# Kernel optimization log

Measured on AMD Instinct MI355X. Metric: run time of the kernel, lower is better.

## Reference

```python
import jax, jax.numpy as jnp
import numpy as np

B, D, C = 16384, 512, 1000  # batch, feature dim, number of class prototypes


def setup_inputs() -> dict:
    key = jax.random.key(0)
    kx, kp = jax.random.split(key)
    x = jax.random.normal(kx, (B, D), dtype=jnp.float32)
    protomat = jax.random.normal(kp, (C, D), dtype=jnp.float32)
    return {"x": x, "protomat": protomat}


def reference(x, protomat):
    # Squared L2 distance from every sample to every prototype:
    # dist[b, c] = sum_d (x[b,d] - protomat[c,d])^2
    # materializing the [B, C, D] broadcast the original loop implies.
    x_sq = jnp.sum(x * x, axis=1, keepdims=True)            # [B, 1]
    p_sq = jnp.sum(protomat * protomat, axis=1)             # [C]
    cross = jnp.einsum('bd,cd->bc', x, protomat)            # [B, C]
    return x_sq + p_sq[None, :] - 2.0 * cross               # [B, C]
```

## Files before the change

kernel.cpp:

```cpp
#include <hip/hip_runtime.h>
#include <hip/hip_bf16.h>


#define B_ROWS 16384
#define D_K    512
#define C_COLS 1000
#define C_PAD  1024

#define BM 128
#define BN 128
#define BK 32

typedef __attribute__((ext_vector_type(8))) short short8;
typedef __attribute__((ext_vector_type(4))) float f32x4;

__device__ __forceinline__ unsigned short f2bf(float f) {
  unsigned u = __float_as_uint(f);
  u += 0x7fffu + ((u >> 16) & 1u);
  return (unsigned short)(u >> 16);
}

__device__ __forceinline__ void gload16(const void* g, void* l) {
  __builtin_amdgcn_global_load_lds(
      (const __attribute__((address_space(1))) unsigned int*)g,
      (__attribute__((address_space(3))) unsigned int*)l, 16, 0, 0);
}

__global__ __launch_bounds__(256) void prep_kernel(
    const float* __restrict__ x, const float* __restrict__ p,
    unsigned short* __restrict__ xb, unsigned short* __restrict__ pb,
    float* __restrict__ xsq, float* __restrict__ psq) {
  const int wave = threadIdx.x >> 6;
  const int lane = threadIdx.x & 63;
  const int row  = blockIdx.x * 4 + wave;
  const bool isx = row < B_ROWS;
  const int r2   = isx ? row : row - B_ROWS;

  float v[8];
  if (isx) {
    const float4* s = reinterpret_cast<const float4*>(x + (size_t)r2 * D_K + lane * 8);
    float4 a = s[0], b = s[1];
    v[0] = a.x; v[1] = a.y; v[2] = a.z; v[3] = a.w;
    v[4] = b.x; v[5] = b.y; v[6] = b.z; v[7] = b.w;
  } else if (r2 < C_COLS) {
    const float4* s = reinterpret_cast<const float4*>(p + (size_t)r2 * D_K + lane * 8);
    float4 a = s[0], b = s[1];
    v[0] = a.x; v[1] = a.y; v[2] = a.z; v[3] = a.w;
    v[4] = b.x; v[5] = b.y; v[6] = b.z; v[7] = b.w;
  } else {
#pragma unroll
    for (int j = 0; j < 8; ++j) v[j] = 0.0f;
  }

  float ss = 0.0f;
  unsigned short u[8];
#pragma unroll
  for (int j = 0; j < 8; ++j) { ss += v[j] * v[j]; u[j] = f2bf(v[j]); }

  uint4 pk;
  pk.x = (unsigned)u[0] | ((unsigned)u[1] << 16);
  pk.y = (unsigned)u[2] | ((unsigned)u[3] << 16);
  pk.z = (unsigned)u[4] | ((unsigned)u[5] << 16);
  pk.w = (unsigned)u[6] | ((unsigned)u[7] << 16);
  unsigned short* dst = (isx ? xb : pb) + (size_t)r2 * D_K + lane * 8;
  *reinterpret_cast<uint4*>(dst) = pk;

#pragma unroll
  for (int off = 32; off > 0; off >>= 1) ss += __shfl_down(ss, off);
  if (lane == 0) (isx ? xsq : psq)[r2] = ss;
}

__global__ __launch_bounds__(256, 2) void gemm_kernel(
    const unsigned short* __restrict__ xb, const unsigned short* __restrict__ pb,
    const float* __restrict__ xsq, const float* __restrict__ psq,
    float* __restrict__ out) {
  __shared__ __align__(16) unsigned short As[BM * BK];
  __shared__ __align__(16) unsigned short Bs[BN * BK];

  const int tid  = threadIdx.x;
  const int lane = tid & 63;
  const int wave = tid >> 6;
  const int wr   = wave >> 1;
  const int wc   = wave & 1;
  const int bm   = blockIdx.y;
  const int bn   = blockIdx.x;

  const int ch0 = tid;
  const int ch1 = tid + 256;
  const unsigned short* a0 = xb + ((size_t)bm * BM + (ch0 >> 2)) * D_K + (ch0 & 3) * 8;
  const unsigned short* a1 = xb + ((size_t)bm * BM + (ch1 >> 2)) * D_K + (ch1 & 3) * 8;
  const unsigned short* b0 = pb + ((size_t)bn * BN + (ch0 >> 2)) * D_K + (ch0 & 3) * 8;
  const unsigned short* b1 = pb + ((size_t)bn * BN + (ch1 >> 2)) * D_K + (ch1 & 3) * 8;
  unsigned short* la0 = &As[ch0 * 8];
  unsigned short* la1 = &As[ch1 * 8];
  unsigned short* lb0 = &Bs[ch0 * 8];
  unsigned short* lb1 = &Bs[ch1 * 8];

  f32x4 acc[4][4];
#pragma unroll
  for (int i = 0; i < 4; ++i)
#pragma unroll
    for (int j = 0; j < 4; ++j) acc[i][j] = (f32x4){0.f, 0.f, 0.f, 0.f};

  const int mrow = wr * 64 + (lane & 15);
  const int ncol = wc * 64 + (lane & 15);
  const int koff = (lane >> 4) * 8;

#pragma unroll 1
  for (int ks = 0; ks < D_K / BK; ++ks) {
    const int ko = ks * BK;
    gload16(a0 + ko, la0);
    gload16(a1 + ko, la1);
    gload16(b0 + ko, lb0);
    gload16(b1 + ko, lb1);
    __syncthreads();

    short8 af[4], bf[4];
#pragma unroll
    for (int i = 0; i < 4; ++i)
      af[i] = *reinterpret_cast<const short8*>(&As[(mrow + i * 16) * BK + koff]);
#pragma unroll
    for (int j = 0; j < 4; ++j)
      bf[j] = *reinterpret_cast<const short8*>(&Bs[(ncol + j * 16) * BK + koff]);

#pragma unroll
    for (int i = 0; i < 4; ++i)
#pragma unroll
      for (int j = 0; j < 4; ++j)
        acc[i][j] = __builtin_amdgcn_mfma_f32_16x16x32_bf16(af[i], bf[j], acc[i][j], 0, 0, 0);

    __syncthreads();
  }

  const int colbase = bn * BN + wc * 64 + (lane & 15);
  float pc[4];
#pragma unroll
  for (int j = 0; j < 4; ++j) pc[j] = psq[colbase + j * 16];

  const int rowbase = bm * BM + wr * 64 + ((lane >> 4) << 2);
#pragma unroll
  for (int i = 0; i < 4; ++i) {
#pragma unroll
    for (int r = 0; r < 4; ++r) {
      const int row = rowbase + i * 16 + r;
      const float xs = xsq[row];
#pragma unroll
      for (int j = 0; j < 4; ++j) {
        const int c = colbase + j * 16;
        if (c < C_COLS)
          out[(size_t)row * C_COLS + c] = xs + pc[j] - 2.0f * acc[i][j][r];
      }
    }
  }
}

extern "C" void kernel_launch(void* const* d_in, const int* in_sizes, int n_in,
                              void* d_out, int out_size, void* d_ws, size_t ws_size,
                              hipStream_t stream) {
  const float* x = (const float*)d_in[0];
  const float* p = (const float*)d_in[1];
  float* out = (float*)d_out;

  char* ws = (char*)d_ws;
  unsigned short* xb  = (unsigned short*)ws;
  unsigned short* pb  = (unsigned short*)(ws + 16777216);
  float* xsq          = (float*)(ws + 16777216 + 1048576);
  float* psq          = (float*)(ws + 16777216 + 1048576 + 65536);

  prep_kernel<<<(B_ROWS + C_PAD) / 4, 256, 0, stream>>>(x, p, xb, pb, xsq, psq);

  dim3 grid(C_PAD / BN, B_ROWS / BM, 1);
  gemm_kernel<<<grid, 256, 0, stream>>>(xb, pb, xsq, psq, out);
}
```

Before: 123.4 us.

## Fuse bf16 conversion and norms into a single double-buffered 256x256 GEMM kernel

Drops the separate prep kernel and workspace round-trip. The GEMM now loads fp32 x and prototypes straight from global memory into registers, converts them to bf16, accumulates squared norms on the fly and writes swizzled LDS tiles through a register-prefetched double buffer. Tiles grow to 256x256 with 512 threads, and the grid is a remapped 1D grid of 256 blocks. In exchange, the prototype operand is converted redundantly in every block, occupancy drops to one large block per CU, and only 256 blocks are launched.

```diff
diff --git a/kernel.cpp b/kernel.cpp
--- a/kernel.cpp
+++ b/kernel.cpp
@@ -5,150 +5,141 @@
 #define B_ROWS 16384
 #define D_K    512
 #define C_COLS 1000
-#define C_PAD  1024
 
-#define BM 128
-#define BN 128
+#define BM 256
+#define BN 256
 #define BK 32
+#define NTL (D_K / BK)
 
 typedef __attribute__((ext_vector_type(8))) short short8;
 typedef __attribute__((ext_vector_type(4))) float f32x4;
 
-__device__ __forceinline__ unsigned short f2bf(float f) {
-  unsigned u = __float_as_uint(f);
-  u += 0x7fffu + ((u >> 16) & 1u);
-  return (unsigned short)(u >> 16);
+__device__ __forceinline__ f32x4 MFMA(short8 a, short8 b, f32x4 c) {
+  return __builtin_amdgcn_mfma_f32_16x16x32_bf16(a, b, c, 0, 0, 0);
 }
 
-__device__ __forceinline__ void gload16(const void* g, void* l) {
-  __builtin_amdgcn_global_load_lds(
-      (const __attribute__((address_space(1))) unsigned int*)g,
-      (__attribute__((address_space(3))) unsigned int*)l, 16, 0, 0);
-}
-
-__global__ __launch_bounds__(256) void prep_kernel(
+__global__ __launch_bounds__(512, 1) void fused_kernel(
     const float* __restrict__ x, const float* __restrict__ p,
-    unsigned short* __restrict__ xb, unsigned short* __restrict__ pb,
-    float* __restrict__ xsq, float* __restrict__ psq) {
-  const int wave = threadIdx.x >> 6;
-  const int lane = threadIdx.x & 63;
-  const int row  = blockIdx.x * 4 + wave;
-  const bool isx = row < B_ROWS;
-  const int r2   = isx ? row : row - B_ROWS;
-
-  float v[8];
-  if (isx) {
-    const float4* s = reinterpret_cast<const float4*>(x + (size_t)r2 * D_K + lane * 8);
-    float4 a = s[0], b = s[1];
-    v[0] = a.x; v[1] = a.y; v[2] = a.z; v[3] = a.w;
-    v[4] = b.x; v[5] = b.y; v[6] = b.z; v[7] = b.w;
-  } else if (r2 < C_COLS) {
-    const float4* s = reinterpret_cast<const float4*>(p + (size_t)r2 * D_K + lane * 8);
-    float4 a = s[0], b = s[1];
-    v[0] = a.x; v[1] = a.y; v[2] = a.z; v[3] = a.w;
-    v[4] = b.x; v[5] = b.y; v[6] = b.z; v[7] = b.w;
-  } else {
-#pragma unroll
-    for (int j = 0; j < 8; ++j) v[j] = 0.0f;
-  }
-
-  float ss = 0.0f;
-  unsigned short u[8];
-#pragma unroll
-  for (int j = 0; j < 8; ++j) { ss += v[j] * v[j]; u[j] = f2bf(v[j]); }
-
-  uint4 pk;
-  pk.x = (unsigned)u[0] | ((unsigned)u[1] << 16);
-  pk.y = (unsigned)u[2] | ((unsigned)u[3] << 16);
-  pk.z = (unsigned)u[4] | ((unsigned)u[5] << 16);
-  pk.w = (unsigned)u[6] | ((unsigned)u[7] << 16);
-  unsigned short* dst = (isx ? xb : pb) + (size_t)r2 * D_K + lane * 8;
-  *reinterpret_cast<uint4*>(dst) = pk;
-
-#pragma unroll
-  for (int off = 32; off > 0; off >>= 1) ss += __shfl_down(ss, off);
-  if (lane == 0) (isx ? xsq : psq)[r2] = ss;
-}
-
-__global__ __launch_bounds__(256, 2) void gemm_kernel(
-    const unsigned short* __restrict__ xb, const unsigned short* __restrict__ pb,
-    const float* __restrict__ xsq, const float* __restrict__ psq,
     float* __restrict__ out) {
-  __shared__ __align__(16) unsigned short As[BM * BK];
-  __shared__ __align__(16) unsigned short Bs[BN * BK];
+  __shared__ __align__(16) unsigned short L[2 * 16384];
+  __shared__ float SQ[512];
 
   const int tid  = threadIdx.x;
   const int lane = tid & 63;
   const int wave = tid >> 6;
-  const int wr   = wave >> 1;
-  const int wc   = wave & 1;
-  const int bm   = blockIdx.y;
-  const int bn   = blockIdx.x;
+  const int wm   = wave >> 2;
+  const int wn   = wave & 3;
 
-  const int ch0 = tid;
-  const int ch1 = tid + 256;
-  const unsigned short* a0 = xb + ((size_t)bm * BM + (ch0 >> 2)) * D_K + (ch0 & 3) * 8;
-  const unsigned short* a1 = xb + ((size_t)bm * BM + (ch1 >> 2)) * D_K + (ch1 & 3) * 8;
-  const unsigned short* b0 = pb + ((size_t)bn * BN + (ch0 >> 2)) * D_K + (ch0 & 3) * 8;
-  const unsigned short* b1 = pb + ((size_t)bn * BN + (ch1 >> 2)) * D_K + (ch1 & 3) * 8;
-  unsigned short* la0 = &As[ch0 * 8];
-  unsigned short* la1 = &As[ch1 * 8];
-  unsigned short* lb0 = &Bs[ch0 * 8];
-  unsigned short* lb1 = &Bs[ch1 * 8];
+  const int bid = blockIdx.x;
+  const int tt  = (bid & 7) * 32 + (bid >> 3);
+  const int bm  = tt >> 2;
+  const int bn  = tt & 3;
 
-  f32x4 acc[4][4];
+  const int rloc = tid & 255;
+  const float* gsrc;
+  if (tid < 256) {
+    gsrc = x + (size_t)(bm * BM + rloc) * D_K;
+  } else {
+    int prow = bn * BN + rloc;
+    if (prow > C_COLS - 1) prow = C_COLS - 1;
+    gsrc = p + (size_t)prow * D_K;
+  }
+  unsigned short* lreg = L + (tid < 256 ? 0 : 8192);
+  const int rsh = (rloc >> 1) & 3;
+
+  float ssq = 0.f;
+  float4 RA[8], RB[8];
+
+  auto GLOAD = [&](float4* R, int T) {
+    const float4* s = reinterpret_cast<const float4*>(gsrc + T * BK);
 #pragma unroll
-  for (int i = 0; i < 4; ++i)
+    for (int j = 0; j < 8; ++j) R[j] = s[j];
+  };
+
+  auto CVTW = [&](const float4* R, int BUF) {
+    __hip_bfloat162 h[16];
 #pragma unroll
-    for (int j = 0; j < 4; ++j) acc[i][j] = (f32x4){0.f, 0.f, 0.f, 0.f};
+    for (int j = 0; j < 8; ++j) {
+      ssq += R[j].x * R[j].x + R[j].y * R[j].y + R[j].z * R[j].z +
+             R[j].w * R[j].w;
+      h[2 * j]     = __float22bfloat162_rn(float2{R[j].x, R[j].y});
+      h[2 * j + 1] = __float22bfloat162_rn(float2{R[j].z, R[j].w});
+    }
+    const uint4* hu = reinterpret_cast<const uint4*>(h);
+    unsigned short* base = lreg + BUF * 16384;
+#pragma unroll
+    for (int ks = 0; ks < 4; ++ks) {
+      const int chunk = rloc * 4 + ((ks + rsh) & 3);
+      *reinterpret_cast<uint4*>(base + chunk * 8) = hu[ks];
+    }
+  };
 
-  const int mrow = wr * 64 + (lane & 15);
-  const int ncol = wc * 64 + (lane & 15);
-  const int koff = (lane >> 4) * 8;
+  f32x4 acc[8][4];
+#pragma unroll
+  for (int m = 0; m < 8; ++m)
+#pragma unroll
+    for (int n = 0; n < 4; ++n) acc[m][n] = (f32x4){0.f, 0.f, 0.f, 0.f};
+
+  const int l15  = lane & 15;
+  const int posL = (((lane >> 4) + (l15 >> 1)) & 3);
+  const int rdA  = (wm * 128 + l15) * 32 + posL * 8;
+  const int rdB  = 8192 + (wn * 64 + l15) * 32 + posL * 8;
+
+  auto COMPUTE = [&](int BUF) {
+    const unsigned short* Ab = &L[BUF * 16384] + rdA;
+    const unsigned short* Bb = &L[BUF * 16384] + rdB;
+    short8 bfr[4];
+#pragma unroll
+    for (int n = 0; n < 4; ++n)
+      bfr[n] = *reinterpret_cast<const short8*>(Bb + n * 512);
+    __builtin_amdgcn_s_setprio(1);
+#pragma unroll
+    for (int m = 0; m < 8; ++m) {
+      short8 af = *reinterpret_cast<const short8*>(Ab + m * 512);
+#pragma unroll
+      for (int n = 0; n < 4; ++n) acc[m][n] = MFMA(af, bfr[n], acc[m][n]);
+    }
+    __builtin_amdgcn_s_setprio(0);
+  };
+
+  GLOAD(RA, 0);
+  GLOAD(RB, 1);
+  CVTW(RA, 0);
+  __syncthreads();
 
 #pragma unroll 1
-  for (int ks = 0; ks < D_K / BK; ++ks) {
-    const int ko = ks * BK;
-    gload16(a0 + ko, la0);
-    gload16(a1 + ko, la1);
-    gload16(b0 + ko, lb0);
-    gload16(b1 + ko, lb1);
+  for (int t = 0; t < NTL; t += 2) {
+    if (t + 2 < NTL) GLOAD(RA, t + 2);
+    COMPUTE(0);
+    CVTW(RB, 1);
     __syncthreads();
-
-    short8 af[4], bf[4];
-#pragma unroll
-    for (int i = 0; i < 4; ++i)
-      af[i] = *reinterpret_cast<const short8*>(&As[(mrow + i * 16) * BK + koff]);
-#pragma unroll
-    for (int j = 0; j < 4; ++j)
-      bf[j] = *reinterpret_cast<const short8*>(&Bs[(ncol + j * 16) * BK + koff]);
-
-#pragma unroll
-    for (int i = 0; i < 4; ++i)
-#pragma unroll
-      for (int j = 0; j < 4; ++j)
-        acc[i][j] = __builtin_amdgcn_mfma_f32_16x16x32_bf16(af[i], bf[j], acc[i][j], 0, 0, 0);
-
+    if (t + 3 < NTL) GLOAD(RB, t + 3);
+    COMPUTE(1);
+    if (t + 2 < NTL) CVTW(RA, 0);
     __syncthreads();
   }
 
-  const int colbase = bn * BN + wc * 64 + (lane & 15);
+  SQ[tid] = ssq;
+  __syncthreads();
+
+  const int col_l = wn * 64 + l15;
   float pc[4];
 #pragma unroll
-  for (int j = 0; j < 4; ++j) pc[j] = psq[colbase + j * 16];
+  for (int n = 0; n < 4; ++n) pc[n] = SQ[256 + col_l + n * 16];
 
-  const int rowbase = bm * BM + wr * 64 + ((lane >> 4) << 2);
+  const int row_l0 = wm * 128 + ((lane >> 4) << 2);
+  const int gcol0  = bn * BN + col_l;
 #pragma unroll
-  for (int i = 0; i < 4; ++i) {
+  for (int m = 0; m < 8; ++m) {
 #pragma unroll
     for (int r = 0; r < 4; ++r) {
-      const int row = rowbase + i * 16 + r;
-      const float xs = xsq[row];
+      const int row_l = row_l0 + m * 16 + r;
+      const float xs  = SQ[row_l];
+      const size_t gr = (size_t)(bm * BM + row_l) * C_COLS;
 #pragma unroll
-      for (int j = 0; j < 4; ++j) {
-        const int c = colbase + j * 16;
-        if (c < C_COLS)
-          out[(size_t)row * C_COLS + c] = xs + pc[j] - 2.0f * acc[i][j][r];
+      for (int n = 0; n < 4; ++n) {
+        const int c = gcol0 + n * 16;
+        if (c < C_COLS) out[gr + c] = xs + pc[n] - 2.0f * acc[m][n][r];
       }
     }
   }
@@ -161,14 +152,5 @@
   const float* p = (const float*)d_in[1];
   float* out = (float*)d_out;
 
-  char* ws = (char*)d_ws;
-  unsigned short* xb  = (unsigned short*)ws;
-  unsigned short* pb  = (unsigned short*)(ws + 16777216);
-  float* xsq          = (float*)(ws + 16777216 + 1048576);
-  float* psq          = (float*)(ws + 16777216 + 1048576 + 65536);
-
-  prep_kernel<<<(B_ROWS + C_PAD) / 4, 256, 0, stream>>>(x, p, xb, pb, xsq, psq);
-
-  dim3 grid(C_PAD / BN, B_ROWS / BM, 1);
-  gemm_kernel<<<grid, 256, 0, stream>>>(xb, pb, xsq, psq, out);
+  fused_kernel<<<256, 512, 0, stream>>>(x, p, out);
 }
```

After: 143.5 us. 16.2% more time.
